# Performance work log

Hardware: AMD Instinct MI355X
Metric: run time of the kernel (lower is better)

Reference implementation:

```python
import jax, jax.numpy as jnp
import numpy as np

P = 2  # sampling ratio: keep top ceil(M/p) measurements


def setup_inputs() -> dict:
    key = jax.random.key(0)
    k1, k2, k3 = jax.random.split(key, 3)
    B, H, W, C = 8, 1024, 1024, 3
    Y = jax.random.normal(k1, (B, H, W, C), dtype=jnp.float32)
    # build()-time Z0 components: abs ~ N(0.5, 0.1), angle ~ N(0, 0.5*sqrt(pi))
    Z0_abs = 0.5 + 0.1 * jax.random.normal(k2, (1, 1, H, W), dtype=jnp.float32)
    Z0_angle = (0.5 * np.pi ** 0.5) * jax.random.normal(k3, (1, 1, H, W), dtype=jnp.float32)
    return {"Y": Y, "Z0_abs": Z0_abs, "Z0_angle": Z0_angle}


def _make_Z0(Z0_abs, Z0_angle):
    # Z0 = |Z0| * exp(i*angle), Frobenius-normalized over spatial axes (2,3)
    Z0 = Z0_abs.astype(jnp.complex64) * jnp.exp(1j * Z0_angle.astype(jnp.complex64))
    fro = jnp.sqrt(jnp.sum(jnp.abs(Z0) ** 2, axis=(2, 3), keepdims=True)).astype(jnp.complex64)
    return Z0 / fro


def reference(Y, Z0_abs, Z0_angle):
    B, H, W, C = Y.shape
    M = H * W * C
    R = int(np.ceil(M / P))
    # transpose NHWC -> NCHW, scale by original S[2] (= W)
    Y_S = jnp.transpose(Y.astype(jnp.float32), (0, 3, 1, 2)) / jnp.float32(W)
    y_s = Y_S.reshape(B, M)
    # threshold = R-th largest value per batch (== descending-sorted index R-1)
    thr = jax.lax.top_k(y_s, R)[0][:, -1]  # [B]
    Ytr = (Y_S >= thr[:, None, None, None]).astype(jnp.float32)  # [B,C,H,W]
    Z0 = _make_Z0(Z0_abs, Z0_angle)
    return Ytr, Z0
```

## Files before the change

### kernel.cpp

```cpp
#include <hip/hip_runtime.h>
#include <math.h>

#define BATCH 8
#define HH 1024
#define WW 1024
#define CC 3
#define MTOT (HH*WW*CC)
#define RSEL 1572864u
#define NSEG 96
#define SEGCAP 3072u

#define U_HI 0xBC800000u
#define U_LO 0x437FFFFFu

#define WS_SCNT_OFF   0u
#define WS_CHI_OFF    4096u
#define WS_NPART_OFF  8192u
#define WS_THR_OFF    12288u
#define WS_NORM_OFF   12352u
#define WS_BUF_OFF    16384u

__device__ __forceinline__ unsigned int fmap(float x) {
    unsigned int b = __float_as_uint(x);
    return (b & 0x80000000u) ? ~b : (b | 0x80000000u);
}

__global__ void pass1_kernel(const float* __restrict__ Y,
                             const float* __restrict__ zabs,
                             unsigned int* __restrict__ buf,
                             unsigned int* __restrict__ scnt,
                             unsigned int* __restrict__ chi,
                             float* __restrict__ npart) {
    const int tid = threadIdx.x;
    const int bx = blockIdx.x;

    if (blockIdx.y == 8) {
        float s = 0.f;
        const int n4z = HH * WW / 4;
        for (int i = bx * blockDim.x + tid; i < n4z; i += NSEG * blockDim.x) {
            float4 v = ((const float4*)zabs)[i];
            s += v.x * v.x + v.y * v.y + v.z * v.z + v.w * v.w;
        }
        for (int d = 32; d > 0; d >>= 1) s += __shfl_down(s, d);
        __shared__ float ls[4];
        if ((tid & 63) == 0) ls[tid >> 6] = s;
        __syncthreads();
        if (tid == 0) npart[bx] = ls[0] + ls[1] + ls[2] + ls[3];
        return;
    }

    __shared__ unsigned int lbuf[2048];
    __shared__ unsigned int lcnt;
    __shared__ unsigned int red[4];
    const int b = blockIdx.y;
    if (tid == 0) lcnt = 0u;
    __syncthreads();

    const float4* Y4 = (const float4*)(Y + (size_t)b * MTOT);
    unsigned int* seg = buf + (size_t)(b * NSEG + bx) * SEGCAP;
    const int n4 = MTOT / 4;
    const int stride = NSEG * blockDim.x;
    const int iters = n4 / stride;
    unsigned int hcnt = 0u;
    unsigned int base = 0u;

    for (int it = 0; it < iters; it++) {
        int i = it * stride + bx * blockDim.x + tid;
        float4 v = Y4[i];
        unsigned int u;
#define PROC(comp) u = fmap(comp); \
        if (u >= U_HI) hcnt++; \
        else if (u >= U_LO) { unsigned int p = atomicAdd(&lcnt, 1u); if (p < 2048u) lbuf[p] = u; }
        PROC(v.x) PROC(v.y) PROC(v.z) PROC(v.w)
#undef PROC
        __syncthreads();
        unsigned int n = lcnt;
        if (n >= 1024u) {
            for (unsigned int j = tid; j < n; j += blockDim.x) {
                unsigned int p = base + j;
                if (p < SEGCAP) seg[p] = lbuf[j];
            }
            base += n;
            __syncthreads();
            if (tid == 0) lcnt = 0u;
        }
        __syncthreads();
    }
    unsigned int n = lcnt;
    if (n > 2048u) n = 2048u;
    for (unsigned int j = tid; j < n; j += blockDim.x) {
        unsigned int p = base + j;
        if (p < SEGCAP) seg[p] = lbuf[j];
    }
    base += lcnt;
    if (tid == 0) scnt[b * NSEG + bx] = base;

    for (int d = 32; d > 0; d >>= 1) hcnt += __shfl_down(hcnt, d);
    if ((tid & 63) == 0) red[tid >> 6] = hcnt;
    __syncthreads();
    if (tid == 0) chi[b * NSEG + bx] = red[0] + red[1] + red[2] + red[3];
}

__global__ void __launch_bounds__(1024) refine_kernel(
        const float* __restrict__ Y,
        const unsigned int* __restrict__ buf,
        const unsigned int* __restrict__ scnt,
        const unsigned int* __restrict__ chi,
        const float* __restrict__ npart,
        unsigned int* __restrict__ thr,
        float* __restrict__ normsum) {
    const int tid = threadIdx.x;

    if (blockIdx.x == 8) {
        if (tid == 0) {
            float s = 0.f;
            for (int i = 0; i < NSEG; i++) s += npart[i];
            *normsum = s;
        }
        return;
    }

    __shared__ unsigned int hist[4096];
    __shared__ unsigned int segcnt[NSEG];
    __shared__ unsigned int waveSums[16];
    __shared__ unsigned int selBin, selBase;
    __shared__ unsigned int mode_s, target_s;
    const int b = blockIdx.x;
    const int lane = tid & 63, wid = tid >> 6;

    if (tid < NSEG) {
        unsigned int c = scnt[b * NSEG + tid];
        segcnt[tid] = (c > SEGCAP) ? SEGCAP : c;
    }
    if (tid == 0) {
        unsigned int tot = 0u, Ch = 0u, mx = 0u;
        for (int j = 0; j < NSEG; j++) {
            unsigned int c = scnt[b * NSEG + j];
            if (c > mx) mx = c;
            tot += c;
            Ch += chi[b * NSEG + j];
        }
        int fb = (mx > SEGCAP) || (Ch >= RSEL) || (Ch + tot < RSEL);
        mode_s = (unsigned int)fb;
        target_s = fb ? RSEL : (RSEL - Ch);
    }
    __syncthreads();
    const int fb = (int)mode_s;
    unsigned int target = target_s;
    const unsigned int* bseg = buf + (size_t)b * NSEG * SEGCAP;
    const float* Yb = Y + (size_t)b * MTOT;

    unsigned int d1 = 0, d2 = 0;

    for (int level = 0; level < 3; level++) {
        const int nb  = (level < 2) ? 4096 : 256;
        const int bpt = (level < 2) ? 4 : 1;
        for (int i = tid; i < nb; i += 1024) hist[i] = 0u;
        if (tid == 0) { selBin = 0u; selBase = 0u; }
        __syncthreads();

#define HISTO(u) do { \
            if (level == 0) atomicAdd(&hist[(u) >> 20], 1u); \
            else if (level == 1) { if (((u) >> 20) == d1) atomicAdd(&hist[((u) >> 8) & 0xFFFu], 1u); } \
            else { if (((u) >> 8) == ((d1 << 12) | d2)) atomicAdd(&hist[(u) & 0xFFu], 1u); } \
        } while (0)

        if (fb) {
            for (unsigned int i = tid; i < (unsigned int)MTOT; i += 1024u) {
                unsigned int u = fmap(Yb[i]);
                HISTO(u);
            }
        } else {
            for (int sj = wid; sj < NSEG; sj += 16) {
                const unsigned int cj = segcnt[sj];
                const unsigned int* sp = bseg + (size_t)sj * SEGCAP;
                for (unsigned int k = lane; k < cj; k += 64u) {
                    unsigned int u = sp[k];
                    HISTO(u);
                }
            }
        }
#undef HISTO
        __syncthreads();
        unsigned int c[4] = {0u, 0u, 0u, 0u};
        unsigned int s = 0u;
        const int nthr = nb / bpt;
        if (tid < nthr)
            for (int k = 0; k < bpt; k++) { c[k] = hist[nb - 1 - (tid * bpt + k)]; s += c[k]; }
        unsigned int incl = s;
        for (int d = 1; d < 64; d <<= 1) {
            unsigned int v = __shfl_up(incl, d);
            if (lane >= d) incl += v;
        }
        if (lane == 63) waveSums[wid] = incl;
        __syncthreads();
        if (tid < 16) {
            unsigned int w = waveSums[tid];
            for (int d = 1; d < 16; d <<= 1) {
                unsigned int v = __shfl_up(w, d);
                if (tid >= d) w += v;
            }
            waveSums[tid] = w;
        }
        __syncthreads();
        incl += (wid > 0) ? waveSums[wid - 1] : 0u;
        unsigned int excl = incl - s;
        if (s > 0u && excl < target && incl >= target) {
            unsigned int run = excl;
            for (int k = 0; k < bpt; k++) {
                if (run + c[k] >= target) {
                    selBin = (unsigned int)(nb - 1 - (tid * bpt + k));
                    selBase = run;
                    break;
                }
                run += c[k];
            }
        }
        __syncthreads();
        if (level == 0) d1 = selBin;
        else if (level == 1) d2 = selBin;
        target -= selBase;
        __syncthreads();
    }
    if (tid == 0) thr[b] = (d1 << 20) | (d2 << 8) | selBin;
}

__global__ void thresh_z_kernel(const float* __restrict__ Y,
                                const unsigned int* __restrict__ thr,
                                const float* __restrict__ zabs,
                                const float* __restrict__ zang,
                                const float* __restrict__ normsum,
                                float* __restrict__ out,
                                float* __restrict__ outz, int interleaved) {
    if (blockIdx.x < 8192) {
        int p = blockIdx.x * blockDim.x + threadIdx.x;
        int w4 = p & 255;
        int h  = (p >> 8) & 1023;
        int b  = p >> 18;
        unsigned int tu = thr[b];
        const float4* src = (const float4*)(Y + ((size_t)((b * HH + h) * WW) + (size_t)w4 * 4) * CC);
        float4 a0 = src[0], a1 = src[1], a2 = src[2];
        float4 r0, r1, r2;
        r0.x = (fmap(a0.x) >= tu) ? 1.f : 0.f;
        r0.y = (fmap(a0.w) >= tu) ? 1.f : 0.f;
        r0.z = (fmap(a1.z) >= tu) ? 1.f : 0.f;
        r0.w = (fmap(a2.y) >= tu) ? 1.f : 0.f;
        r1.x = (fmap(a0.y) >= tu) ? 1.f : 0.f;
        r1.y = (fmap(a1.x) >= tu) ? 1.f : 0.f;
        r1.z = (fmap(a1.w) >= tu) ? 1.f : 0.f;
        r1.w = (fmap(a2.z) >= tu) ? 1.f : 0.f;
        r2.x = (fmap(a0.z) >= tu) ? 1.f : 0.f;
        r2.y = (fmap(a1.y) >= tu) ? 1.f : 0.f;
        r2.z = (fmap(a2.x) >= tu) ? 1.f : 0.f;
        r2.w = (fmap(a2.w) >= tu) ? 1.f : 0.f;
        size_t base = ((size_t)(b * CC) * HH + h) * WW;
        ((float4*)(out + base))[w4]                        = r0;
        ((float4*)(out + base + (size_t)HH * WW))[w4]      = r1;
        ((float4*)(out + base + (size_t)2 * HH * WW))[w4]  = r2;
    } else {
        int i = (blockIdx.x - 8192) * blockDim.x + threadIdx.x;
        float inv = 1.0f / sqrtf(*normsum);
        float2 a = ((const float2*)zabs)[i];
        float2 g = ((const float2*)zang)[i];
        float s0, c0, s1, c1;
        __sincosf(g.x, &s0, &c0);
        __sincosf(g.y, &s1, &c1);
        if (interleaved) {
            float4 o;
            o.x = a.x * c0 * inv; o.y = a.x * s0 * inv;
            o.z = a.y * c1 * inv; o.w = a.y * s1 * inv;
            ((float4*)outz)[i] = o;
        } else {
            float2 o;
            o.x = a.x * c0 * inv; o.y = a.y * c1 * inv;
            ((float2*)outz)[i] = o;
        }
    }
}

extern "C" void kernel_launch(void* const* d_in, const int* in_sizes, int n_in,
                              void* d_out, int out_size, void* d_ws, size_t ws_size,
                              hipStream_t stream) {
    const float* Y    = (const float*)d_in[0];
    const float* zabs = (const float*)d_in[1];
    const float* zang = (const float*)d_in[2];
    float* out = (float*)d_out;

    unsigned char* ws = (unsigned char*)d_ws;
    unsigned int* scnt  = (unsigned int*)(ws + WS_SCNT_OFF);
    unsigned int* chi   = (unsigned int*)(ws + WS_CHI_OFF);
    float*        npart = (float*)(ws + WS_NPART_OFF);
    unsigned int* thr   = (unsigned int*)(ws + WS_THR_OFF);
    float*        norm  = (float*)(ws + WS_NORM_OFF);
    unsigned int* buf   = (unsigned int*)(ws + WS_BUF_OFF);

    dim3 g1(NSEG, 9);
    pass1_kernel<<<g1, 256, 0, stream>>>(Y, zabs, buf, scnt, chi, npart);
    refine_kernel<<<9, 1024, 0, stream>>>(Y, buf, scnt, chi, npart, thr, norm);

    size_t zoff = (size_t)BATCH * CC * HH * WW;
    int zfloats = out_size - (int)zoff;
    int interleaved = (zfloats >= 2 * HH * WW) ? 1 : 0;
    thresh_z_kernel<<<8192 + 2048, 256, 0, stream>>>(
        Y, thr, zabs, zang, norm, out, out + zoff, interleaved);
}
```

Baseline: 244.1 us.

## Widen pass1 grid and compact candidates into per-batch global buffers via atomics

```diff
diff --git a/kernel.cpp b/kernel.cpp
--- a/kernel.cpp
+++ b/kernel.cpp
@@ -7,18 +7,20 @@
 #define CC 3
 #define MTOT (HH*WW*CC)
 #define RSEL 1572864u
-#define NSEG 96
-#define SEGCAP 3072u
+
+#define NSEG2 256
+#define LCAP 1024u
+#define WCAP 131072u
 
 #define U_HI 0xBC800000u
 #define U_LO 0x437FFFFFu
 
-#define WS_SCNT_OFF   0u
-#define WS_CHI_OFF    4096u
-#define WS_NPART_OFF  8192u
-#define WS_THR_OFF    12288u
-#define WS_NORM_OFF   12352u
-#define WS_BUF_OFF    16384u
+#define WS_WCNT_OFF  0u
+#define WS_CHI_OFF   64u
+#define WS_NPART_OFF 256u
+#define WS_THR_OFF   2048u
+#define WS_NORM_OFF  2112u
+#define WS_WBUF_OFF  4096u
 
 __device__ __forceinline__ unsigned int fmap(float x) {
     unsigned int b = __float_as_uint(x);
@@ -27,9 +29,9 @@
 
 __global__ void pass1_kernel(const float* __restrict__ Y,
                              const float* __restrict__ zabs,
-                             unsigned int* __restrict__ buf,
-                             unsigned int* __restrict__ scnt,
-                             unsigned int* __restrict__ chi,
+                             unsigned int* __restrict__ wbuf,
+                             unsigned int* __restrict__ wcnt,
+                             unsigned int* __restrict__ chib,
                              float* __restrict__ npart) {
     const int tid = threadIdx.x;
     const int bx = blockIdx.x;
@@ -37,7 +39,7 @@
     if (blockIdx.y == 8) {
         float s = 0.f;
         const int n4z = HH * WW / 4;
-        for (int i = bx * blockDim.x + tid; i < n4z; i += NSEG * blockDim.x) {
+        for (int i = bx * 256 + tid; i < n4z; i += NSEG2 * 256) {
             float4 v = ((const float4*)zabs)[i];
             s += v.x * v.x + v.y * v.y + v.z * v.z + v.w * v.w;
         }
@@ -49,105 +51,91 @@
         return;
     }
 
-    __shared__ unsigned int lbuf[2048];
+    __shared__ unsigned int lbuf[LCAP];
     __shared__ unsigned int lcnt;
     __shared__ unsigned int red[4];
+    __shared__ unsigned int gbase_s;
     const int b = blockIdx.y;
     if (tid == 0) lcnt = 0u;
     __syncthreads();
 
     const float4* Y4 = (const float4*)(Y + (size_t)b * MTOT);
-    unsigned int* seg = buf + (size_t)(b * NSEG + bx) * SEGCAP;
-    const int n4 = MTOT / 4;
-    const int stride = NSEG * blockDim.x;
-    const int iters = n4 / stride;
+    const int stride = NSEG2 * 256;
     unsigned int hcnt = 0u;
-    unsigned int base = 0u;
-
-    for (int it = 0; it < iters; it++) {
-        int i = it * stride + bx * blockDim.x + tid;
-        float4 v = Y4[i];
-        unsigned int u;
-#define PROC(comp) u = fmap(comp); \
+
+#define PROC(c) do { unsigned int u = fmap(c); \
         if (u >= U_HI) hcnt++; \
-        else if (u >= U_LO) { unsigned int p = atomicAdd(&lcnt, 1u); if (p < 2048u) lbuf[p] = u; }
-        PROC(v.x) PROC(v.y) PROC(v.z) PROC(v.w)
+        else if (u >= U_LO) { unsigned int p = atomicAdd(&lcnt, 1u); if (p < LCAP) lbuf[p] = u; } \
+    } while (0)
+#define PROC4(v) do { PROC(v.x); PROC(v.y); PROC(v.z); PROC(v.w); } while (0)
+
+    for (int it = 0; it < 12; it += 4) {
+        int i0 = it * stride + bx * 256 + tid;
+        float4 v0 = Y4[i0];
+        float4 v1 = Y4[i0 + stride];
+        float4 v2 = Y4[i0 + 2 * stride];
+        float4 v3 = Y4[i0 + 3 * stride];
+        PROC4(v0); PROC4(v1); PROC4(v2); PROC4(v3);
+    }
+#undef PROC4
 #undef PROC
-        __syncthreads();
-        unsigned int n = lcnt;
-        if (n >= 1024u) {
-            for (unsigned int j = tid; j < n; j += blockDim.x) {
-                unsigned int p = base + j;
-                if (p < SEGCAP) seg[p] = lbuf[j];
-            }
-            base += n;
-            __syncthreads();
-            if (tid == 0) lcnt = 0u;
-        }
-        __syncthreads();
-    }
+
+    __syncthreads();
     unsigned int n = lcnt;
-    if (n > 2048u) n = 2048u;
-    for (unsigned int j = tid; j < n; j += blockDim.x) {
-        unsigned int p = base + j;
-        if (p < SEGCAP) seg[p] = lbuf[j];
-    }
-    base += lcnt;
-    if (tid == 0) scnt[b * NSEG + bx] = base;
-
+    unsigned int nc = (n > LCAP) ? LCAP : n;
+    if (tid == 0) {
+        unsigned int add = (n > LCAP) ? (WCAP + 1u) : n;
+        gbase_s = atomicAdd(&wcnt[b], add);
+    }
     for (int d = 32; d > 0; d >>= 1) hcnt += __shfl_down(hcnt, d);
     if ((tid & 63) == 0) red[tid >> 6] = hcnt;
     __syncthreads();
-    if (tid == 0) chi[b * NSEG + bx] = red[0] + red[1] + red[2] + red[3];
+    if (tid == 0) atomicAdd(&chib[b], red[0] + red[1] + red[2] + red[3]);
+
+    unsigned int gbase = gbase_s;
+    unsigned int* wb = wbuf + (size_t)b * WCAP;
+    for (unsigned int j = tid; j < nc; j += 256u) {
+        unsigned int p = gbase + j;
+        if (p < WCAP) wb[p] = lbuf[j];
+    }
 }
 
 __global__ void __launch_bounds__(1024) refine_kernel(
         const float* __restrict__ Y,
-        const unsigned int* __restrict__ buf,
-        const unsigned int* __restrict__ scnt,
-        const unsigned int* __restrict__ chi,
+        const unsigned int* __restrict__ wbuf,
+        const unsigned int* __restrict__ wcnt,
+        const unsigned int* __restrict__ chib,
         const float* __restrict__ npart,
         unsigned int* __restrict__ thr,
         float* __restrict__ normsum) {
     const int tid = threadIdx.x;
 
     if (blockIdx.x == 8) {
+        float s = (tid < NSEG2) ? npart[tid] : 0.f;
+        for (int d = 32; d > 0; d >>= 1) s += __shfl_down(s, d);
+        __shared__ float ls[16];
+        if ((tid & 63) == 0) ls[tid >> 6] = s;
+        __syncthreads();
         if (tid == 0) {
-            float s = 0.f;
-            for (int i = 0; i < NSEG; i++) s += npart[i];
-            *normsum = s;
+            float t = 0.f;
+            for (int i = 0; i < 16; i++) t += ls[i];
+            *normsum = t;
         }
         return;
     }
 
     __shared__ unsigned int hist[4096];
-    __shared__ unsigned int segcnt[NSEG];
     __shared__ unsigned int waveSums[16];
     __shared__ unsigned int selBin, selBase;
-    __shared__ unsigned int mode_s, target_s;
     const int b = blockIdx.x;
     const int lane = tid & 63, wid = tid >> 6;
 
-    if (tid < NSEG) {
-        unsigned int c = scnt[b * NSEG + tid];
-        segcnt[tid] = (c > SEGCAP) ? SEGCAP : c;
-    }
-    if (tid == 0) {
-        unsigned int tot = 0u, Ch = 0u, mx = 0u;
-        for (int j = 0; j < NSEG; j++) {
-            unsigned int c = scnt[b * NSEG + j];
-            if (c > mx) mx = c;
-            tot += c;
-            Ch += chi[b * NSEG + j];
-        }
-        int fb = (mx > SEGCAP) || (Ch >= RSEL) || (Ch + tot < RSEL);
-        mode_s = (unsigned int)fb;
-        target_s = fb ? RSEL : (RSEL - Ch);
-    }
-    __syncthreads();
-    const int fb = (int)mode_s;
-    unsigned int target = target_s;
-    const unsigned int* bseg = buf + (size_t)b * NSEG * SEGCAP;
+    const unsigned int wc = wcnt[b];
+    const unsigned int Ch = chib[b];
+    const int fb = (wc > WCAP) || (Ch >= RSEL) || (Ch + wc < RSEL);
+    unsigned int target = fb ? RSEL : (RSEL - Ch);
+    const unsigned int wcg = (wc > WCAP) ? WCAP : wc;
+    const unsigned int* wp = wbuf + (size_t)b * WCAP;
     const float* Yb = Y + (size_t)b * MTOT;
 
     unsigned int d1 = 0, d2 = 0;
@@ -171,13 +159,9 @@
                 HISTO(u);
             }
         } else {
-            for (int sj = wid; sj < NSEG; sj += 16) {
-                const unsigned int cj = segcnt[sj];
-                const unsigned int* sp = bseg + (size_t)sj * SEGCAP;
-                for (unsigned int k = lane; k < cj; k += 64u) {
-                    unsigned int u = sp[k];
-                    HISTO(u);
-                }
+            for (unsigned int i = tid; i < wcg; i += 1024u) {
+                unsigned int u = wp[i];
+                HISTO(u);
             }
         }
 #undef HISTO
@@ -287,16 +271,18 @@
     float* out = (float*)d_out;
 
     unsigned char* ws = (unsigned char*)d_ws;
-    unsigned int* scnt  = (unsigned int*)(ws + WS_SCNT_OFF);
-    unsigned int* chi   = (unsigned int*)(ws + WS_CHI_OFF);
+    unsigned int* wcnt  = (unsigned int*)(ws + WS_WCNT_OFF);
+    unsigned int* chib  = (unsigned int*)(ws + WS_CHI_OFF);
     float*        npart = (float*)(ws + WS_NPART_OFF);
     unsigned int* thr   = (unsigned int*)(ws + WS_THR_OFF);
     float*        norm  = (float*)(ws + WS_NORM_OFF);
-    unsigned int* buf   = (unsigned int*)(ws + WS_BUF_OFF);
-
-    dim3 g1(NSEG, 9);
-    pass1_kernel<<<g1, 256, 0, stream>>>(Y, zabs, buf, scnt, chi, npart);
-    refine_kernel<<<9, 1024, 0, stream>>>(Y, buf, scnt, chi, npart, thr, norm);
+    unsigned int* wbuf  = (unsigned int*)(ws + WS_WBUF_OFF);
+
+    hipMemsetAsync(ws, 0, 96, stream);
+
+    dim3 g1(NSEG2, 9);
+    pass1_kernel<<<g1, 256, 0, stream>>>(Y, zabs, wbuf, wcnt, chib, npart);
+    refine_kernel<<<9, 1024, 0, stream>>>(Y, wbuf, wcnt, chib, npart, thr, norm);
 
     size_t zoff = (size_t)BATCH * CC * HH * WW;
     int zfloats = out_size - (int)zoff;
```

Result: no change. 241.7 us (-1.0%).
